# Optimization experiments

Hardware: AMD Instinct MI355X
Metric: run time of the kernel (lower is better)

Reference implementation:

```python
import jax, jax.numpy as jnp
import numpy as np

N = 50000
E = 1600000
IN_C = 128
HEADS = 4
OUT_C = 16


def setup_inputs() -> dict:
    key = jax.random.key(0)
    ks = jax.random.split(key, 8)
    x = jax.random.normal(ks[0], (N, IN_C), dtype=jnp.float32)
    edge_index = jax.random.randint(ks[1], (2, E), 0, N, dtype=jnp.int64)
    W = jax.random.normal(ks[2], (IN_C, HEADS * OUT_C), dtype=jnp.float32) * (1.0 / np.sqrt(IN_C))
    att_src = jax.random.normal(ks[3], (HEADS, OUT_C), dtype=jnp.float32) * 0.1
    att_dst = jax.random.normal(ks[4], (HEADS, OUT_C), dtype=jnp.float32) * 0.1
    bias_gat = jnp.zeros((HEADS * OUT_C,), dtype=jnp.float32)
    W_out = jax.random.normal(ks[5], (HEADS * OUT_C, 1), dtype=jnp.float32) * (1.0 / np.sqrt(HEADS * OUT_C))
    b_out = jnp.zeros((1,), dtype=jnp.float32)
    return {"x": x, "edge_index": edge_index, "W": W, "att_src": att_src,
            "att_dst": att_dst, "bias_gat": bias_gat, "W_out": W_out, "b_out": b_out}


def reference(x, edge_index, W, att_src, att_dst, bias_gat, W_out, b_out):
    n = x.shape[0]
    # Linear projection, reshape to [N, H, C]
    xw = (x @ W).reshape(n, HEADS, OUT_C)
    # Per-node attention logits: [N, H]
    a_src = jnp.einsum('nhc,hc->nh', xw, att_src)
    a_dst = jnp.einsum('nhc,hc->nh', xw, att_dst)
    src, dst = edge_index[0], edge_index[1]
    # Per-edge raw scores with leaky relu (PyG negative_slope=0.2): [E, H]
    alpha = jax.nn.leaky_relu(a_src[src] + a_dst[dst], negative_slope=0.2)
    # Segment softmax over incoming edges of each destination node
    amax = jax.ops.segment_max(alpha, dst, num_segments=n)  # [N, H]
    ex = jnp.exp(alpha - amax[dst])
    denom = jax.ops.segment_sum(ex, dst, num_segments=n)  # [N, H]
    attn = ex / (denom[dst] + 1e-16)  # [E, H]
    # Weighted scatter-add aggregation: [N, H, C]
    msg = xw[src] * attn[:, :, None]
    agg = jax.ops.segment_sum(msg, dst, num_segments=n)
    out = agg.reshape(n, HEADS * OUT_C) + bias_gat
    out = jax.nn.elu(out)
    y = out @ W_out + b_out  # [N, 1]
    return y.squeeze(-1)
```

## Files before the change

kernel.cpp:

```cpp
#include <hip/hip_runtime.h>
#include <hip/hip_fp16.h>

#define NNODES 50000
#define INC 128
#define HC 64
#define NHEADS 4
#define NBUCK 196
#define NB_A 512
#define PB_CAP 10240
#define PROJ_P 200
#define NTILES 3125
#define WLD 80

typedef _Float16 f16x8 __attribute__((ext_vector_type(8)));
typedef float f32x4 __attribute__((ext_vector_type(4)));

__global__ __launch_bounds__(256) void proj_count_kernel(
    const float* __restrict__ x, const float* __restrict__ W,
    const float* __restrict__ att_s, const float* __restrict__ att_d,
    const int* __restrict__ ei,
    _Float16* __restrict__ xw_h, float* __restrict__ a_src,
    float* __restrict__ a_dst, int* __restrict__ cnt_mat, int E)
{
    __shared__ _Float16 Wh[INC * WLD];
    const int t = threadIdx.x;

    if (blockIdx.x < PROJ_P) {
        if (t < INC) {
            const float* wr = W + t * HC;
            _Float16* dst = Wh + t * WLD;
            float sa0=0,sa1=0,sa2=0,sa3=0, sd0=0,sd1=0,sd2=0,sd3=0;
            #pragma unroll 16
            for (int c = 0; c < 16; ++c) {
                const float w0 = wr[c], w1 = wr[16+c], w2 = wr[32+c], w3 = wr[48+c];
                dst[c] = (_Float16)w0; dst[16+c] = (_Float16)w1;
                dst[32+c] = (_Float16)w2; dst[48+c] = (_Float16)w3;
                sa0 = fmaf(w0, att_s[c],    sa0); sd0 = fmaf(w0, att_d[c],    sd0);
                sa1 = fmaf(w1, att_s[16+c], sa1); sd1 = fmaf(w1, att_d[16+c], sd1);
                sa2 = fmaf(w2, att_s[32+c], sa2); sd2 = fmaf(w2, att_d[32+c], sd2);
                sa3 = fmaf(w3, att_s[48+c], sa3); sd3 = fmaf(w3, att_d[48+c], sd3);
            }
            dst[64] = (_Float16)sa0; dst[65] = (_Float16)sa1;
            dst[66] = (_Float16)sa2; dst[67] = (_Float16)sa3;
            dst[68] = (_Float16)sd0; dst[69] = (_Float16)sd1;
            dst[70] = (_Float16)sd2; dst[71] = (_Float16)sd3;
        }
        __syncthreads();

        const int w = t >> 6, lane = t & 63;
        const int r16 = lane & 15, g = lane >> 4;

        f16x8 bf[5][4];
        #pragma unroll
        for (int ct = 0; ct < 5; ++ct)
            #pragma unroll
            for (int kt = 0; kt < 4; ++kt)
                #pragma unroll
                for (int j = 0; j < 8; ++j)
                    bf[ct][kt][j] = Wh[(kt * 32 + g * 8 + j) * WLD + ct * 16 + r16];

        for (int tile = blockIdx.x * 4 + w; tile < NTILES; tile += PROJ_P * 4) {
            const int n0 = tile * 16;
            const float* xrow = x + (size_t)(n0 + r16) * INC + g * 8;
            f16x8 af[4];
            #pragma unroll
            for (int kt = 0; kt < 4; ++kt) {
                const float4 v0 = *reinterpret_cast<const float4*>(xrow + kt * 32);
                const float4 v1 = *reinterpret_cast<const float4*>(xrow + kt * 32 + 4);
                af[kt][0] = (_Float16)v0.x; af[kt][1] = (_Float16)v0.y;
                af[kt][2] = (_Float16)v0.z; af[kt][3] = (_Float16)v0.w;
                af[kt][4] = (_Float16)v1.x; af[kt][5] = (_Float16)v1.y;
                af[kt][6] = (_Float16)v1.z; af[kt][7] = (_Float16)v1.w;
            }
            f32x4 acc[5];
            #pragma unroll
            for (int ct = 0; ct < 5; ++ct) acc[ct] = (f32x4){0.f, 0.f, 0.f, 0.f};
            #pragma unroll
            for (int ct = 0; ct < 5; ++ct)
                #pragma unroll
                for (int kt = 0; kt < 4; ++kt)
                    acc[ct] = __builtin_amdgcn_mfma_f32_16x16x32_f16(
                        af[kt], bf[ct][kt], acc[ct], 0, 0, 0);

            #pragma unroll
            for (int ct = 0; ct < 4; ++ct)
                #pragma unroll
                for (int r = 0; r < 4; ++r)
                    xw_h[(size_t)(n0 + g * 4 + r) * HC + ct * 16 + r16] =
                        (_Float16)acc[ct][r];
            #pragma unroll
            for (int r = 0; r < 4; ++r) {
                const int n = n0 + g * 4 + r;
                if (r16 < 4)       a_src[n * NHEADS + r16]       = acc[4][r];
                else if (r16 < 8)  a_dst[n * NHEADS + (r16 - 4)] = acc[4][r];
            }
        }
    } else {
        int* lh = (int*)Wh;
        const int blk = blockIdx.x - PROJ_P;
        for (int i = t; i < NBUCK; i += 256) lh[i] = 0;
        __syncthreads();
        const int chunk = (E + NB_A - 1) / NB_A;
        const int beg = blk * chunk;
        const int end = (beg + chunk < E) ? beg + chunk : E;
        for (int i = beg + t; i < end; i += 256)
            atomicAdd(&lh[((unsigned)ei[E + i]) >> 8], 1);
        __syncthreads();
        for (int i = t; i < NBUCK; i += 256)
            cnt_mat[blk * NBUCK + i] = lh[i];
    }
}

__global__ __launch_bounds__(256) void scan_all_kernel(
    const int* __restrict__ cnt_mat, int* __restrict__ offs_mat,
    int* __restrict__ btotal, int* __restrict__ gbase)
{
    __shared__ int sc[256];
    const int t = threadIdx.x;

    int tot = 0;
    if (t < NBUCK)
        for (int k = 0; k < NB_A; ++k) tot += cnt_mat[k * NBUCK + t];
    sc[t] = tot;
    __syncthreads();
    for (int off = 1; off < 256; off <<= 1) {
        const int u = (t >= off) ? sc[t - off] : 0;
        __syncthreads();
        sc[t] += u;
        __syncthreads();
    }
    if (t < NBUCK) {
        btotal[t] = tot;
        int run = sc[t] - tot;
        gbase[t] = run;
        for (int k = 0; k < NB_A; ++k) {
            offs_mat[k * NBUCK + t] = run;
            run += cnt_mat[k * NBUCK + t];
        }
    }
}

__global__ __launch_bounds__(512) void binA_write(
    const int* __restrict__ ei, const int* __restrict__ offs_mat,
    unsigned* __restrict__ payload, int E)
{
    __shared__ int cur[NBUCK];
    const int t = threadIdx.x, blk = blockIdx.x;
    for (int b = t; b < NBUCK; b += 512)
        cur[b] = offs_mat[blk * NBUCK + b];
    __syncthreads();
    const int chunk = (E + NB_A - 1) / NB_A;
    const int beg = blk * chunk;
    const int end = (beg + chunk < E) ? beg + chunk : E;
    for (int i = beg + t; i < end; i += 512) {
        const unsigned s = (unsigned)ei[i];
        const unsigned d = (unsigned)ei[E + i];
        const int pos = atomicAdd(&cur[d >> 8], 1);
        payload[pos] = (s << 16) | d;
    }
}

__global__ __launch_bounds__(512) void passB_kernel(
    const int* __restrict__ btotal, const int* __restrict__ gbase,
    unsigned* __restrict__ payload, int* __restrict__ rowptr)
{
    __shared__ unsigned pl[PB_CAP];
    __shared__ int lh[256];
    __shared__ int sc[256];
    const int b = blockIdx.x, t = threadIdx.x;
    const int base = gbase[b];
    int ecnt = btotal[b]; if (ecnt > PB_CAP) ecnt = PB_CAP;

    for (int i = t; i < ecnt; i += 512) pl[i] = payload[base + i];
    if (t < 256) lh[t] = 0;
    __syncthreads();
    for (int i = t; i < ecnt; i += 512) atomicAdd(&lh[pl[i] & 255], 1);
    __syncthreads();

    const int val = (t < 256) ? lh[t] : 0;
    if (t < 256) sc[t] = val;
    __syncthreads();
    for (int off = 1; off < 256; off <<= 1) {
        const int u = (t >= off && t < 256) ? sc[t - off] : 0;
        __syncthreads();
        if (t < 256) sc[t] += u;
        __syncthreads();
    }
    if (t < 256) {
        const int excl = sc[t] - val;
        const int node = b * 256 + t;
        if (node <= NNODES) rowptr[node] = base + excl;
        lh[t] = excl;
    }
    __syncthreads();

    for (int i = t; i < ecnt; i += 512) {
        const unsigned p = pl[i];
        const int pos = atomicAdd(&lh[p & 255], 1);
        payload[base + pos] = p >> 16;
    }
}

__global__ __launch_bounds__(256) void agg_kernel(
    const int* __restrict__ rowptr, const unsigned* __restrict__ sorted_src,
    const __half* __restrict__ xw_h, const float* __restrict__ a_src,
    const float* __restrict__ a_dst, const float* __restrict__ bias,
    const float* __restrict__ Wo, const float* __restrict__ bo,
    float* __restrict__ y)
{
    const int lane = threadIdx.x & 63;
    const int g = lane >> 4;
    const int q = lane & 15;
    const int h = q >> 2;
    const int n = blockIdx.x * 4 + (threadIdx.x >> 6);

    const int beg = rowptr[n], end = rowptr[n + 1];
    const float ad = a_dst[n * NHEADS + h];

    float ax = 0.f, ay = 0.f, az = 0.f, aw = 0.f;
    float den = 0.f;
    #pragma unroll 2
    for (int i = beg; i < end; i += 4) {
        const int idx = i + g;
        const int s = (int)sorted_src[idx < end ? idx : end - 1];
        const float av = a_src[s * NHEADS + h] + ad;
        float ex = __expf(fmaxf(av, 0.2f * av));
        if (idx >= end) ex = 0.f;
        den += ex;
        const uint2 u = *reinterpret_cast<const uint2*>(xw_h + (size_t)s * HC + q * 4);
        const __half2 h01 = __builtin_bit_cast(__half2, u.x);
        const __half2 h23 = __builtin_bit_cast(__half2, u.y);
        const float2 f01 = __half22float2(h01);
        const float2 f23 = __half22float2(h23);
        ax = fmaf(ex, f01.x, ax);
        ay = fmaf(ex, f01.y, ay);
        az = fmaf(ex, f23.x, az);
        aw = fmaf(ex, f23.y, aw);
    }
    #pragma unroll
    for (int off = 16; off <= 32; off <<= 1) {
        ax  += __shfl_xor(ax, off, 64);
        ay  += __shfl_xor(ay, off, 64);
        az  += __shfl_xor(az, off, 64);
        aw  += __shfl_xor(aw, off, 64);
        den += __shfl_xor(den, off, 64);
    }
    const float inv = 1.f / (den + 1e-16f);
    const float4 bi = *reinterpret_cast<const float4*>(&bias[q * 4]);
    const float4 wo = *reinterpret_cast<const float4*>(&Wo[q * 4]);
    float v, p = 0.f;
    v = ax * inv + bi.x; p += (v > 0.f ? v : __expf(v) - 1.f) * wo.x;
    v = ay * inv + bi.y; p += (v > 0.f ? v : __expf(v) - 1.f) * wo.y;
    v = az * inv + bi.z; p += (v > 0.f ? v : __expf(v) - 1.f) * wo.z;
    v = aw * inv + bi.w; p += (v > 0.f ? v : __expf(v) - 1.f) * wo.w;
    p += __shfl_xor(p, 1, 64);
    p += __shfl_xor(p, 2, 64);
    p += __shfl_xor(p, 4, 64);
    p += __shfl_xor(p, 8, 64);
    if (lane == 0) y[n] = p + bo[0];
}

extern "C" void kernel_launch(void* const* d_in, const int* in_sizes, int n_in,
                              void* d_out, int out_size, void* d_ws, size_t ws_size,
                              hipStream_t stream) {
    const float* x     = (const float*)d_in[0];
    const int*   ei    = (const int*)d_in[1];
    const float* W     = (const float*)d_in[2];
    const float* att_s = (const float*)d_in[3];
    const float* att_d = (const float*)d_in[4];
    const float* bias  = (const float*)d_in[5];
    const float* Wo    = (const float*)d_in[6];
    const float* bo    = (const float*)d_in[7];
    float*       y     = (float*)d_out;

    const int E = in_sizes[1] / 2;

    char* wsb = (char*)d_ws;
    _Float16* xw_h    = (_Float16*)wsb;
    float*    a_src   = (float*)(wsb + 6400000);
    float*    a_dst   = (float*)(wsb + 7200000);
    unsigned* payload = (unsigned*)(wsb + 8000000);
    int*      rowptr  = (int*)(wsb + 14400000);
    int*      cnt_mat = (int*)(wsb + 14600256);
    int*      offs_mat= (int*)(wsb + 15001664);
    int*      btotal  = (int*)(wsb + 15403072);
    int*      gbase   = (int*)(wsb + 15403904);

    proj_count_kernel<<<PROJ_P + NB_A, 256, 0, stream>>>(
        x, W, att_s, att_d, ei, xw_h, a_src, a_dst, cnt_mat, E);
    scan_all_kernel<<<1, 256, 0, stream>>>(cnt_mat, offs_mat, btotal, gbase);
    binA_write<<<NB_A, 512, 0, stream>>>(ei, offs_mat, payload, E);
    passB_kernel<<<NBUCK, 512, 0, stream>>>(btotal, gbase, payload, rowptr);
    agg_kernel<<<NNODES / 4, 256, 0, stream>>>(rowptr, payload,
                                               (const __half*)xw_h, a_src,
                                               a_dst, bias, Wo, bo, y);
}
```

Baseline: 190.7 us.

## Transpose bucket count matrix and parallelize scan across 1024 threads

The per-block bucket count matrix is stored bucket-major, so one flat exclusive scan over all entries yields both per-block offsets and per-bucket bases. The single-block scan kernel now uses 1024 threads, each summing and writing a contiguous chunk, where before 196 threads each walked a strided column serially. The number of histogram/binning blocks is halved, which shortens the scan but gives each block more edges to handle in the count and write passes. Bucket totals are derived from adjacent offsets and E.

```diff
diff --git a/kernel.cpp b/kernel.cpp
--- a/kernel.cpp
+++ b/kernel.cpp
@@ -6,7 +6,7 @@
 #define HC 64
 #define NHEADS 4
 #define NBUCK 196
-#define NB_A 512
+#define NB_A 256
 #define PB_CAP 10240
 #define PROJ_P 200
 #define NTILES 3125
@@ -107,36 +107,42 @@
             atomicAdd(&lh[((unsigned)ei[E + i]) >> 8], 1);
         __syncthreads();
         for (int i = t; i < NBUCK; i += 256)
-            cnt_mat[blk * NBUCK + i] = lh[i];
-    }
-}
-
-__global__ __launch_bounds__(256) void scan_all_kernel(
+            cnt_mat[i * NB_A + blk] = lh[i];
+    }
+}
+
+__global__ __launch_bounds__(1024) void scan_all_kernel(
     const int* __restrict__ cnt_mat, int* __restrict__ offs_mat,
-    int* __restrict__ btotal, int* __restrict__ gbase)
-{
-    __shared__ int sc[256];
+    int* __restrict__ btotal, int* __restrict__ gbase, int E)
+{
+    __shared__ int sc[1024];
     const int t = threadIdx.x;
-
-    int tot = 0;
-    if (t < NBUCK)
-        for (int k = 0; k < NB_A; ++k) tot += cnt_mat[k * NBUCK + t];
-    sc[t] = tot;
-    __syncthreads();
-    for (int off = 1; off < 256; off <<= 1) {
+    const int CH = (NBUCK * NB_A) / 1024;
+    const int base = t * CH;
+
+    int s = 0;
+    #pragma unroll 7
+    for (int k = 0; k < CH; ++k) s += cnt_mat[base + k];
+    sc[t] = s;
+    __syncthreads();
+    for (int off = 1; off < 1024; off <<= 1) {
         const int u = (t >= off) ? sc[t - off] : 0;
         __syncthreads();
         sc[t] += u;
         __syncthreads();
     }
-    if (t < NBUCK) {
-        btotal[t] = tot;
-        int run = sc[t] - tot;
-        gbase[t] = run;
-        for (int k = 0; k < NB_A; ++k) {
-            offs_mat[k * NBUCK + t] = run;
-            run += cnt_mat[k * NBUCK + t];
-        }
+    int run = sc[t] - s;
+    #pragma unroll 7
+    for (int k = 0; k < CH; ++k) {
+        offs_mat[base + k] = run;
+        run += cnt_mat[base + k];
+    }
+    __syncthreads();
+    for (int b = t; b < NBUCK; b += 1024) {
+        const int g0 = offs_mat[b * NB_A];
+        const int g1 = (b == NBUCK - 1) ? E : offs_mat[(b + 1) * NB_A];
+        gbase[b] = g0;
+        btotal[b] = g1 - g0;
     }
 }
 
@@ -147,7 +153,7 @@
     __shared__ int cur[NBUCK];
     const int t = threadIdx.x, blk = blockIdx.x;
     for (int b = t; b < NBUCK; b += 512)
-        cur[b] = offs_mat[blk * NBUCK + b];
+        cur[b] = offs_mat[b * NB_A + blk];
     __syncthreads();
     const int chunk = (E + NB_A - 1) / NB_A;
     const int beg = blk * chunk;
@@ -282,13 +288,13 @@
     unsigned* payload = (unsigned*)(wsb + 8000000);
     int*      rowptr  = (int*)(wsb + 14400000);
     int*      cnt_mat = (int*)(wsb + 14600256);
-    int*      offs_mat= (int*)(wsb + 15001664);
-    int*      btotal  = (int*)(wsb + 15403072);
-    int*      gbase   = (int*)(wsb + 15403904);
+    int*      offs_mat= (int*)(wsb + 14800960);
+    int*      btotal  = (int*)(wsb + 15001664);
+    int*      gbase   = (int*)(wsb + 15002448);
 
     proj_count_kernel<<<PROJ_P + NB_A, 256, 0, stream>>>(
         x, W, att_s, att_d, ei, xw_h, a_src, a_dst, cnt_mat, E);
-    scan_all_kernel<<<1, 256, 0, stream>>>(cnt_mat, offs_mat, btotal, gbase);
+    scan_all_kernel<<<1, 1024, 0, stream>>>(cnt_mat, offs_mat, btotal, gbase, E);
     binA_write<<<NB_A, 512, 0, stream>>>(ei, offs_mat, payload, E);
     passB_kernel<<<NBUCK, 512, 0, stream>>>(btotal, gbase, payload, rowptr);
     agg_kernel<<<NNODES / 4, 256, 0, stream>>>(rowptr, payload,
```

Result: faster. 184.1 us (-3.4%).
